# Optimization experiments

Hardware: AMD Instinct MI355X
Metric: run time of the kernel (lower is better)

## Reference

```python
import jax, jax.numpy as jnp
import numpy as np

HEADS = 12
DIM_HEAD = 64
INNER = HEADS * DIM_HEAD  # 768
DIM = 512
KS = 3


def setup_inputs() -> dict:
    key = jax.random.key(0)
    ks = jax.random.split(key, 5)
    B, H, W = 8, 32, 32
    N = H * W + 1  # +1 cls token -> has_cls path
    x = jax.random.normal(ks[0], (B, N, DIM), dtype=jnp.float32)
    w_qkv = jax.random.normal(ks[1], (3 * INNER, DIM), dtype=jnp.float32) * (DIM ** -0.5)
    w_dw = jax.random.normal(ks[2], (DIM, 1, KS, KS), dtype=jnp.float32) * (1.0 / KS)
    w_out = jax.random.normal(ks[3], (DIM, INNER), dtype=jnp.float32) * (INNER ** -0.5)
    b_out = jax.random.normal(ks[4], (DIM,), dtype=jnp.float32) * 0.01
    return {"x": x, "w_qkv": w_qkv, "w_dw": w_dw, "w_out": w_out,
            "b_out": b_out, "h_feat": H, "w_feat": W}


def reference(x, w_qkv, w_dw, w_out, b_out, h_feat, w_feat):
    B, N, C = x.shape
    scale = DIM_HEAD ** -0.5
    # qkv projection (Linear, no bias): torch weight layout (out,in)
    qkv = jnp.einsum('bnc,oc->bno', x, w_qkv)  # (B,N,3*INNER)
    q, k, v = jnp.split(qkv, 3, axis=-1)

    def split_heads(t):
        return t.reshape(B, N, HEADS, DIM_HEAD).transpose(0, 2, 1, 3)  # (B,H,N,d)

    q, k, v = map(split_heads, (q, k, v))
    dots = jnp.einsum('bhid,bhjd->bhij', q, k) * scale
    attn = jax.nn.softmax(dots, axis=-1)
    out_attn = jnp.einsum('bhij,bhjd->bhid', attn, v)
    out_attn = out_attn.transpose(0, 2, 1, 3).reshape(B, N, INNER)

    has_cls = (N == h_feat * w_feat + 1)  # static
    spatial = x[:, 1:, :] if has_cls else x
    spatial_2d = spatial.transpose(0, 2, 1).reshape(B, C, h_feat, w_feat)
    # depthwise conv, padding = ks//2 (SAME for odd ks, stride 1)
    loc = jax.lax.conv_general_dilated(
        spatial_2d, w_dw, window_strides=(1, 1), padding='SAME',
        feature_group_count=C,
        dimension_numbers=('NCHW', 'OIHW', 'NCHW'))
    local_out = loc.reshape(B, C, h_feat * w_feat).transpose(0, 2, 1)  # (B,hw,C)
    if has_cls:
        cls_out = x[:, :1, :INNER]  # C < INNER so this is the full cls token
        local_out = jnp.concatenate([cls_out, local_out], axis=1)  # (B,N,C)
    if local_out.shape[-1] < INNER:
        out = out_attn + jnp.pad(
            local_out, ((0, 0), (0, 0), (0, INNER - local_out.shape[-1])))
    else:
        out = out_attn
    # output Linear (dropout=0 in eval)
    return jnp.einsum('bni,oi->bno', out, w_out) + b_out
```

## Files before the change

kernel.cpp:

```cpp
#include <hip/hip_runtime.h>
#include <hip/hip_bf16.h>
#include <stdint.h>
#include <math.h>

typedef __bf16 bf16;
typedef __bf16 bf16x8 __attribute__((ext_vector_type(8)));
typedef float f32x4 __attribute__((ext_vector_type(4)));
typedef short s4 __attribute__((ext_vector_type(4)));

#define QSCALE 0.1803368801111f


__device__ __forceinline__ void gload_lds16(const void* g, void* l) {
  typedef const __attribute__((address_space(1))) char g_char;
  typedef __attribute__((address_space(3))) char l_char;
  g_char* gp = (g_char*)(uintptr_t)g;
  l_char* lp = (l_char*)(uint32_t)(uintptr_t)l;
  __builtin_amdgcn_global_load_lds(gp, lp, 16, 0, 0);
}

__device__ __forceinline__ float fexp2(float x) {
#if __has_builtin(__builtin_amdgcn_exp2f)
  return __builtin_amdgcn_exp2f(x);
#else
  return exp2f(x);
#endif
}

__device__ __forceinline__ float frcp(float x) {
#if __has_builtin(__builtin_amdgcn_rcpf)
  return __builtin_amdgcn_rcpf(x);
#else
  return 1.f / x;
#endif
}

__device__ __forceinline__ uint32_t pk2(float a, float b) {
  union { bf16 h; unsigned short u; } ua, ub;
  ua.h = (bf16)a; ub.h = (bf16)b;
  return (uint32_t)ua.u | ((uint32_t)ub.u << 16);
}

__device__ __forceinline__ f32x4 pv_mfma(s4 a, s4 b, f32x4 c) {
#if __has_builtin(__builtin_amdgcn_mfma_f32_16x16x16bf16_1k)
  return __builtin_amdgcn_mfma_f32_16x16x16bf16_1k(a, b, c, 0, 0, 0);
#else
  asm volatile("v_mfma_f32_16x16x16_bf16 %0, %1, %2, %0" : "+v"(c) : "v"(a), "v"(b));
  return c;
#endif
}

__global__ __launch_bounds__(256) void k_prep(const float* __restrict__ x,
                                              const float* __restrict__ wqkv,
                                              const float* __restrict__ wout,
                                              bf16* __restrict__ xb, bf16* __restrict__ wqkvb,
                                              bf16* __restrict__ woutb) {
  int i = blockIdx.x * 256 + threadIdx.x;
  const float* src = nullptr;
  bf16* dst = nullptr;
  int q = i;
  bool zero = false;
  if (i < 1064960) {
    if (i < 1049600) src = x; else zero = true;
    dst = xb;
  } else if (i < 1064960 + 294912) {
    q = i - 1064960; src = wqkv; dst = wqkvb;
  } else {
    q = i - (1064960 + 294912); src = wout; dst = woutb;
  }
  float4 v = make_float4(0.f, 0.f, 0.f, 0.f);
  if (!zero) v = *(const float4*)&src[(size_t)q * 4];
  uint2 p;
  p.x = pk2(v.x, v.y);
  p.y = pk2(v.z, v.w);
  *(uint2*)&dst[(size_t)q * 4] = p;
}

template <int EPI, int BM, int BN>
__global__ __launch_bounds__(256) void k_gemm(const bf16* __restrict__ A,
                                              const bf16* __restrict__ Bt, int K,
                                              bf16* __restrict__ q, bf16* __restrict__ kk,
                                              bf16* __restrict__ vt,
                                              const float* __restrict__ bias,
                                              float* __restrict__ out) {
  __shared__ __attribute__((aligned(16))) bf16 sA[2][BM * 32];
  __shared__ __attribute__((aligned(16))) bf16 sB[2][BN * 32];
  constexpr int WROWS = BM / 2, WCOLS = BN / 2;
  constexpr int MF = WROWS / 16, NF = WCOLS / 16;
  const int tid = threadIdx.x;
  const int lane = tid & 63;
  const int w = tid >> 6;
  const int wr = w >> 1, wc = w & 1;
  const int tn = blockIdx.x, tm = blockIdx.y;
  const int l15 = lane & 15, l4 = lane >> 4;

  f32x4 acc[MF][NF] = {};

  const int srow = lane >> 2, schunk = lane & 3;
  const int rA = w * (BM / 4) + srow;
  const bf16* aS = A + ((size_t)(tm * BM + rA)) * K + ((schunk ^ (rA & 3)) * 8);
  const int rB = w * (BN / 4) + srow;
  const bf16* bS = Bt + ((size_t)(tn * BN + rB)) * K + ((schunk ^ (rB & 3)) * 8);

  auto STAGE = [&](int bi, int kt) {
    size_t o = (size_t)kt * 32;
#pragma unroll
    for (int i = 0; i < BM / 64; ++i)
      gload_lds16(aS + (size_t)i * 16 * K + o, &sA[bi][(w * (BM / 4) + i * 16) * 32]);
#pragma unroll
    for (int i = 0; i < BN / 64; ++i)
      gload_lds16(bS + (size_t)i * 16 * K + o, &sB[bi][(w * (BN / 4) + i * 16) * 32]);
  };

  STAGE(0, 0);
  int cur = 0;
  const int Ksteps = K >> 5;
  for (int kt = 0; kt < Ksteps; ++kt) {
    asm volatile("s_waitcnt vmcnt(0)" ::: "memory");
    __builtin_amdgcn_s_barrier();
    __builtin_amdgcn_sched_barrier(0);
    if (kt + 1 < Ksteps) STAGE(cur ^ 1, kt + 1);

    const bf16* a_ = sA[cur];
    const bf16* b_ = sB[cur];
    bf16x8 af[MF], bfr[NF];
#pragma unroll
    for (int mf = 0; mf < MF; ++mf) {
      int row = wr * WROWS + mf * 16 + l15;
      int phys = l4 ^ (row & 3);
      af[mf] = *(const bf16x8*)&a_[row * 32 + phys * 8];
    }
#pragma unroll
    for (int nf = 0; nf < NF; ++nf) {
      int row = wc * WCOLS + nf * 16 + l15;
      int phys = l4 ^ (row & 3);
      bfr[nf] = *(const bf16x8*)&b_[row * 32 + phys * 8];
    }
    __builtin_amdgcn_s_setprio(1);
#pragma unroll
    for (int mf = 0; mf < MF; ++mf)
#pragma unroll
      for (int nf = 0; nf < NF; ++nf)
        acc[mf][nf] =
            __builtin_amdgcn_mfma_f32_16x16x32_bf16(bfr[nf], af[mf], acc[mf][nf], 0, 0, 0);
    __builtin_amdgcn_s_setprio(0);
    cur ^= 1;
  }

  const int RbaseL = tm * BM + wr * WROWS + l15;
  const int CbaseL = tn * BN + wc * WCOLS + l4 * 4;
#pragma unroll
  for (int mf = 0; mf < MF; ++mf) {
    int R = RbaseL + mf * 16;
    if (R >= 8200) continue;
    if (EPI == 0) {
      int b = R / 1025;
      int n = R - b * 1025;
      int kvq = n >> 2, e = n & 3;
#pragma unroll
      for (int nf = 0; nf < NF; ++nf) {
        int Cc0 = CbaseL + nf * 16;
        int seg = (Cc0 >= 1536) ? 2 : (Cc0 >= 768 ? 1 : 0);
        int inner = Cc0 - seg * 768;
        int h = inner >> 6, d0 = inner & 63;
        if (seg == 2) {
          bf16* vb = &vt[(((size_t)(b * 12 + h) * 272 + kvq) * 64 + d0) * 4 + e];
#pragma unroll
          for (int r = 0; r < 4; ++r) vb[r * 4] = (bf16)acc[mf][nf][r];
        } else {
          bf16* dst = seg ? kk : q;
          float scl = seg ? 1.f : QSCALE;
          uint2 p;
          p.x = pk2(acc[mf][nf][0] * scl, acc[mf][nf][1] * scl);
          p.y = pk2(acc[mf][nf][2] * scl, acc[mf][nf][3] * scl);
          *(uint2*)&dst[(((size_t)b * 12 + h) * 1088 + n) * 64 + d0] = p;
        }
      }
    } else {
#pragma unroll
      for (int nf = 0; nf < NF; ++nf) {
        int Cc0 = CbaseL + nf * 16;
        float4 bz = *(const float4*)&bias[Cc0];
        float4 o4;
        o4.x = acc[mf][nf][0] + bz.x;
        o4.y = acc[mf][nf][1] + bz.y;
        o4.z = acc[mf][nf][2] + bz.z;
        o4.w = acc[mf][nf][3] + bz.w;
        *(float4*)&out[(size_t)R * 512 + Cc0] = o4;
      }
    }
  }
}

__global__ __launch_bounds__(256) void k_flash(const bf16* __restrict__ qg,
                                               const bf16* __restrict__ kg,
                                               const bf16* __restrict__ vpg,
                                               const bf16* __restrict__ locb,
                                               bf16* __restrict__ outb) {
  __shared__ __attribute__((aligned(16))) bf16 sK[2][64 * 64];
  __shared__ __attribute__((aligned(16))) bf16 sVP[2][16 * 256];
  const int tid = threadIdx.x, lane = tid & 63, w = tid >> 6;
  const int l15 = lane & 15, l4 = lane >> 4;
  const int wg = blockIdx.x;
  const int logical = (wg & 7) * 204 + (wg >> 3);
  const int bh = logical / 17, qgp = logical - bh * 17;
  const int b = bh / 12, h = bh - b * 12;
  const int srow = lane >> 3, sslot = lane & 7;

  size_t qoff = ((size_t)bh * 1088 + qgp * 64 + w * 16 + l15) * 64 + l4 * 8;
  const bf16x8 qf0 = *(const bf16x8*)&qg[qoff];
  const bf16x8 qf1 = *(const bf16x8*)&qg[qoff + 32];

  float lreg = 0.f;
  f32x4 oa[4] = {};

  const int px0 = (l4 ^ (l15 & 7)) * 8;
  const int px1 = ((4 + l4) ^ (l15 & 7)) * 8;

  const int rowA = w * 16 + srow, rowB = rowA + 8;
  const int clogA = sslot ^ (rowA & 7), clogB = sslot ^ (rowB & 7);
  const bf16* kS1 = kg + ((size_t)bh * 1088 + rowA) * 64 + clogA * 8;
  const bf16* kS2 = kg + ((size_t)bh * 1088 + rowB) * 64 + clogB * 8;
  const bf16* vS1 = vpg + (size_t)bh * 69632 + w * 1024 + lane * 8;
  const bf16* vS2 = vS1 + 512;
  const int kD1 = rowA * 64, kD2 = rowB * 64;
  const int vD1 = w * 1024 + lane * 8, vD2 = vD1 + 512;

  auto STAGE = [&](int bi, int t) {
    size_t o = (size_t)t * 4096;
    gload_lds16(kS1 + o, &sK[bi][kD1]);
    gload_lds16(kS2 + o, &sK[bi][kD2]);
    gload_lds16(vS1 + o, &sVP[bi][vD1]);
    gload_lds16(vS2 + o, &sVP[bi][vD2]);
  };

  STAGE(0, 0);
  int cur = 0;

  for (int t = 0; t < 16; ++t) {
    asm volatile("s_waitcnt vmcnt(0)" ::: "memory");
    __builtin_amdgcn_s_barrier();
    __builtin_amdgcn_sched_barrier(0);
    if (t < 15) STAGE(cur ^ 1, t + 1);

    const bf16* kb_ = sK[cur];
    const bf16* vpb = sVP[cur];

    f32x4 sc[4] = {};
    __builtin_amdgcn_s_setprio(1);
#pragma unroll
    for (int jt = 0; jt < 4; ++jt) {
      bf16x8 a0 = *(const bf16x8*)&kb_[(jt * 16 + l15) * 64 + px0];
      sc[jt] = __builtin_amdgcn_mfma_f32_16x16x32_bf16(a0, qf0, sc[jt], 0, 0, 0);
    }
#pragma unroll
    for (int jt = 0; jt < 4; ++jt) {
      bf16x8 a1 = *(const bf16x8*)&kb_[(jt * 16 + l15) * 64 + px1];
      sc[jt] = __builtin_amdgcn_mfma_f32_16x16x32_bf16(a1, qf1, sc[jt], 0, 0, 0);
    }
    __builtin_amdgcn_s_setprio(0);

    union { uint32_t u[2]; s4 v; } pa[4];
    float lsum = 0.f;
#pragma unroll
    for (int jt = 0; jt < 4; ++jt) {
      float p0 = fexp2(sc[jt][0]);
      float p1 = fexp2(sc[jt][1]);
      float p2 = fexp2(sc[jt][2]);
      float p3 = fexp2(sc[jt][3]);
      lsum += (p0 + p1) + (p2 + p3);
      pa[jt].u[0] = pk2(p0, p1);
      pa[jt].u[1] = pk2(p2, p3);
    }
    lreg += lsum;

    __builtin_amdgcn_s_setprio(1);
#pragma unroll
    for (int jt = 0; jt < 4; ++jt)
#pragma unroll
      for (int db = 0; db < 4; ++db) {
        s4 vf = *(const s4*)&vpb[((jt * 4 + l4) * 64 + db * 16 + l15) * 4];
        oa[db] = pv_mfma(pa[jt].v, vf, oa[db]);
      }
    __builtin_amdgcn_s_setprio(0);
    cur ^= 1;
  }

  {
    const bf16* k1 = kg + ((size_t)bh * 1088 + 1024) * 64;
    bf16x8 kA = *(const bf16x8*)&k1[l4 * 8];
    bf16x8 kB = *(const bf16x8*)&k1[32 + l4 * 8];
    float s = 0.f;
#pragma unroll
    for (int e = 0; e < 8; ++e)
      s += (float)qf0[e] * (float)kA[e] + (float)qf1[e] * (float)kB[e];
    s += __shfl_xor(s, 16);
    s += __shfl_xor(s, 32);
    float p = fexp2(s);
    if (l4 == 0) lreg += p;
    float pr[4];
#pragma unroll
    for (int r = 0; r < 4; ++r) pr[r] = __shfl(p, l4 * 4 + r);
    const bf16* v1 = vpg + (size_t)bh * 69632 + 65536;
#pragma unroll
    for (int db = 0; db < 4; ++db) {
      float vd = (float)v1[(db * 16 + l15) * 4];
#pragma unroll
      for (int r = 0; r < 4; ++r) oa[db][r] += pr[r] * vd;
    }
  }

  float ls = lreg;
  ls += __shfl_xor(ls, 16);
  ls += __shfl_xor(ls, 32);
  float linv = frcp(ls);
#pragma unroll
  for (int r = 0; r < 4; ++r) {
    float ir = __shfl(linv, l4 * 4 + r);
    int n = qgp * 64 + w * 16 + l4 * 4 + r;
    if (n >= 1025) continue;
#pragma unroll
    for (int db = 0; db < 4; ++db) {
      float v = oa[db][r] * ir;
      if (h < 8)
        v += (float)locb[((size_t)b * 1025 + n) * 512 + h * 64 + db * 16 + l15];
      outb[((size_t)b * 1025 + n) * 768 + h * 64 + db * 16 + l15] = (bf16)v;
    }
  }
}

__global__ __launch_bounds__(256) void k_local(const float* __restrict__ x,
                                               const float* __restrict__ wdw,
                                               bf16* __restrict__ locb) {
  const int b = blockIdx.x, y = blockIdx.y, xseg = blockIdx.z;
  const int c = threadIdx.x * 2;
  const int x0 = xseg * 4;
  const bool hm = (y > 0), hp = (y < 31);
  float wa[9], wb[9];
#pragma unroll
  for (int k = 0; k < 9; ++k) {
    wa[k] = wdw[(size_t)c * 9 + k];
    wb[k] = wdw[(size_t)(c + 1) * 9 + k];
  }
  const float* xb = x + ((size_t)b * 1025 + 1) * 512 + c;
  float A0 = 0.f, B0 = 0.f, A1 = 0.f, B1 = 0.f;
  for (int cc = x0 - 1; cc <= x0 + 4; ++cc) {
    float2 v0 = make_float2(0.f, 0.f), v1 = v0, v2 = v0;
    if (cc >= 0 && cc < 32) {
      v1 = *(const float2*)&xb[((size_t)y * 32 + cc) * 512];
      if (hm) v0 = *(const float2*)&xb[((size_t)(y - 1) * 32 + cc) * 512];
      if (hp) v2 = *(const float2*)&xb[((size_t)(y + 1) * 32 + cc) * 512];
    }
    float t0a = v0.x * wa[0] + v1.x * wa[3] + v2.x * wa[6];
    float t1a = v0.x * wa[1] + v1.x * wa[4] + v2.x * wa[7];
    float t2a = v0.x * wa[2] + v1.x * wa[5] + v2.x * wa[8];
    float t0b = v0.y * wb[0] + v1.y * wb[3] + v2.y * wb[6];
    float t1b = v0.y * wb[1] + v1.y * wb[4] + v2.y * wb[7];
    float t2b = v0.y * wb[2] + v1.y * wb[5] + v2.y * wb[8];
    int oc = cc - 1;
    if (oc >= x0 && oc <= x0 + 3) {
      size_t o = ((size_t)b * 1025 + 1 + y * 32 + oc) * 512 + c;
      *(uint32_t*)&locb[o] = pk2(A0 + t2a, A1 + t2b);
    }
    A0 = B0 + t1a; B0 = t0a;
    A1 = B1 + t1b; B1 = t0b;
  }
  if (y == 0 && xseg == 0) {
    float2 xc = *(const float2*)&x[((size_t)b * 1025) * 512 + c];
    *(uint32_t*)&locb[((size_t)b * 1025) * 512 + c] = pk2(xc.x, xc.y);
  }
}

extern "C" void kernel_launch(void* const* d_in, const int* in_sizes, int n_in,
                              void* d_out, int out_size, void* d_ws, size_t ws_size,
                              hipStream_t stream) {
  const float* x = (const float*)d_in[0];
  const float* w_qkv = (const float*)d_in[1];
  const float* w_dw = (const float*)d_in[2];
  const float* w_out = (const float*)d_in[3];
  const float* b_out = (const float*)d_in[4];
  float* out = (float*)d_out;

  char* ws = (char*)d_ws;
  size_t off = 0;
  auto alloc = [&](size_t bytes) {
    char* p = ws + off;
    off = (off + bytes + 255) & ~(size_t)255;
    return p;
  };
  bf16* xb    = (bf16*)alloc((size_t)8320 * 512 * 2);
  bf16* wqkvb = (bf16*)alloc((size_t)2304 * 512 * 2);
  bf16* woutb = (bf16*)alloc((size_t)512 * 768 * 2);
  bf16* qb    = (bf16*)alloc((size_t)96 * 1088 * 64 * 2);
  bf16* kb    = (bf16*)alloc((size_t)96 * 1088 * 64 * 2);
  bf16* vP    = (bf16*)alloc((size_t)96 * 272 * 64 * 4 * 2);
  bf16* locb  = (bf16*)alloc((size_t)8 * 1025 * 512 * 2);
  bf16* outb  = (bf16*)alloc((size_t)8320 * 768 * 2);

  k_prep<<<5696, 256, 0, stream>>>(x, w_qkv, w_out, xb, wqkvb, woutb);
  k_gemm<0, 128, 128><<<dim3(18, 65), 256, 0, stream>>>(xb, wqkvb, 512, qb, kb, vP,
                                                        nullptr, nullptr);
  k_local<<<dim3(8, 32, 8), 256, 0, stream>>>(x, w_dw, locb);
  k_flash<<<1632, 256, 0, stream>>>(qb, kb, vP, locb, outb);
  k_gemm<1, 64, 64><<<dim3(8, 130), 256, 0, stream>>>(outb, woutb, 768, nullptr, nullptr,
                                                      nullptr, b_out, out);
}
```

Measured before the change: 142.4 us.

## Triple-buffer GEMM loads, remap blocks per XCD, and change LDS swizzle

The GEMM kernels move from double to triple LDS buffering: loads are issued two k-steps ahead, and a partial vmcnt wait replaces the full drain each iteration. The 2D grid becomes 1D, with a logical tile index remapped so consecutive tiles land on the same XCD for L2 locality. The LDS XOR swizzle now uses (row>>1)&3 to cut bank conflicts on the 16-byte fragment reads. LDS use rises by half, which may lower occupancy slightly.

```diff
diff --git a/kernel.cpp b/kernel.cpp
--- a/kernel.cpp
+++ b/kernel.cpp
@@ -76,31 +76,38 @@
   *(uint2*)&dst[(size_t)q * 4] = p;
 }
 
-template <int EPI, int BM, int BN>
+template <int EPI, int BM, int BN, int NTN>
 __global__ __launch_bounds__(256) void k_gemm(const bf16* __restrict__ A,
                                               const bf16* __restrict__ Bt, int K,
                                               bf16* __restrict__ q, bf16* __restrict__ kk,
                                               bf16* __restrict__ vt,
                                               const float* __restrict__ bias,
                                               float* __restrict__ out) {
-  __shared__ __attribute__((aligned(16))) bf16 sA[2][BM * 32];
-  __shared__ __attribute__((aligned(16))) bf16 sB[2][BN * 32];
+  __shared__ __attribute__((aligned(16))) bf16 sA[3][BM * 32];
+  __shared__ __attribute__((aligned(16))) bf16 sB[3][BN * 32];
   constexpr int WROWS = BM / 2, WCOLS = BN / 2;
   constexpr int MF = WROWS / 16, NF = WCOLS / 16;
+  constexpr int LOADS = BM / 64 + BN / 64;
   const int tid = threadIdx.x;
   const int lane = tid & 63;
   const int w = tid >> 6;
   const int wr = w >> 1, wc = w & 1;
-  const int tn = blockIdx.x, tm = blockIdx.y;
   const int l15 = lane & 15, l4 = lane >> 4;
+
+  const int nwg = gridDim.x;
+  const int qq = nwg >> 3, rr = nwg & 7;
+  const int xcd = blockIdx.x & 7, idx = blockIdx.x >> 3;
+  const int logical = (xcd < rr) ? xcd * (qq + 1) + idx
+                                 : rr * (qq + 1) + (xcd - rr) * qq + idx;
+  const int tm = logical / NTN, tn = logical - tm * NTN;
 
   f32x4 acc[MF][NF] = {};
 
   const int srow = lane >> 2, schunk = lane & 3;
   const int rA = w * (BM / 4) + srow;
-  const bf16* aS = A + ((size_t)(tm * BM + rA)) * K + ((schunk ^ (rA & 3)) * 8);
+  const bf16* aS = A + ((size_t)(tm * BM + rA)) * K + ((schunk ^ ((rA >> 1) & 3)) * 8);
   const int rB = w * (BN / 4) + srow;
-  const bf16* bS = Bt + ((size_t)(tn * BN + rB)) * K + ((schunk ^ (rB & 3)) * 8);
+  const bf16* bS = Bt + ((size_t)(tn * BN + rB)) * K + ((schunk ^ ((rB >> 1) & 3)) * 8);
 
   auto STAGE = [&](int bi, int kt) {
     size_t o = (size_t)kt * 32;
@@ -113,13 +120,22 @@
   };
 
   STAGE(0, 0);
+  STAGE(1, 1);
   int cur = 0;
   const int Ksteps = K >> 5;
   for (int kt = 0; kt < Ksteps; ++kt) {
-    asm volatile("s_waitcnt vmcnt(0)" ::: "memory");
+    if (kt + 1 < Ksteps) {
+      if constexpr (LOADS == 4) asm volatile("s_waitcnt vmcnt(4)" ::: "memory");
+      else                      asm volatile("s_waitcnt vmcnt(2)" ::: "memory");
+    } else {
+      asm volatile("s_waitcnt vmcnt(0)" ::: "memory");
+    }
     __builtin_amdgcn_s_barrier();
     __builtin_amdgcn_sched_barrier(0);
-    if (kt + 1 < Ksteps) STAGE(cur ^ 1, kt + 1);
+    if (kt + 2 < Ksteps) {
+      int b2 = cur + 2; if (b2 >= 3) b2 -= 3;
+      STAGE(b2, kt + 2);
+    }
 
     const bf16* a_ = sA[cur];
     const bf16* b_ = sB[cur];
@@ -127,13 +143,13 @@
 #pragma unroll
     for (int mf = 0; mf < MF; ++mf) {
       int row = wr * WROWS + mf * 16 + l15;
-      int phys = l4 ^ (row & 3);
+      int phys = l4 ^ ((row >> 1) & 3);
       af[mf] = *(const bf16x8*)&a_[row * 32 + phys * 8];
     }
 #pragma unroll
     for (int nf = 0; nf < NF; ++nf) {
       int row = wc * WCOLS + nf * 16 + l15;
-      int phys = l4 ^ (row & 3);
+      int phys = l4 ^ ((row >> 1) & 3);
       bfr[nf] = *(const bf16x8*)&b_[row * 32 + phys * 8];
     }
     __builtin_amdgcn_s_setprio(1);
@@ -144,7 +160,7 @@
         acc[mf][nf] =
             __builtin_amdgcn_mfma_f32_16x16x32_bf16(bfr[nf], af[mf], acc[mf][nf], 0, 0, 0);
     __builtin_amdgcn_s_setprio(0);
-    cur ^= 1;
+    ++cur; if (cur >= 3) cur = 0;
   }
 
   const int RbaseL = tm * BM + wr * WROWS + l15;
@@ -398,10 +414,10 @@
   bf16* outb  = (bf16*)alloc((size_t)8320 * 768 * 2);
 
   k_prep<<<5696, 256, 0, stream>>>(x, w_qkv, w_out, xb, wqkvb, woutb);
-  k_gemm<0, 128, 128><<<dim3(18, 65), 256, 0, stream>>>(xb, wqkvb, 512, qb, kb, vP,
-                                                        nullptr, nullptr);
+  k_gemm<0, 128, 128, 18><<<1170, 256, 0, stream>>>(xb, wqkvb, 512, qb, kb, vP,
+                                                    nullptr, nullptr);
   k_local<<<dim3(8, 32, 8), 256, 0, stream>>>(x, w_dw, locb);
   k_flash<<<1632, 256, 0, stream>>>(qb, kb, vP, locb, outb);
-  k_gemm<1, 64, 64><<<dim3(8, 130), 256, 0, stream>>>(outb, woutb, 768, nullptr, nullptr,
-                                                      nullptr, b_out, out);
-}
+  k_gemm<1, 64, 64, 8><<<1040, 256, 0, stream>>>(outb, woutb, 768, nullptr, nullptr,
+                                                 nullptr, b_out, out);
+}
```

Measured after the change: 137.6 us. 3.3% less time.
